# Performance work log

Measured on AMD Instinct MI355X. Metric: run time of the kernel, lower is better.

The kernel has to match this reference:

```python
import jax, jax.numpy as jnp
import numpy as np

# Capsule layer dims (from original CapsNet paper, per module docstring)
O = 10      # n_out_capsules
U = 36      # n_in_capsules_unique (6*6)
S = 32      # n_in_capsules_sharing_per_unique
E = 16      # n_out_features
F = 8       # n_in_features
N = U * S   # n_in_capsules = 1152
ITERS = 3   # n_iterations
B = 256     # batch size


def squash(v, axis):
    norm = jnp.linalg.norm(v, axis=axis, keepdims=True)
    return v * norm / (1.0 + norm ** 2)


def setup_inputs() -> dict:
    key = jax.random.key(0)
    k1, k2 = jax.random.split(key)
    x = jax.random.normal(k1, (B, N, F), dtype=jnp.float32)
    scale = np.float32(np.sqrt(2.0 / (N * F + O * E)))
    # weights: (n_out_capsules, n_in_capsules_unique, n_out_features, n_in_features)
    W = jax.random.normal(k2, (O, U, E, F), dtype=jnp.float32) * scale
    return {"x": x, "W": W}


def reference(x, W):
    b_sz = x.shape[0]
    xs = x.reshape(b_sz, U, S, F)
    # transform: shared weight over the S sharing dim -> (B, O, U, S, E)
    u = jnp.einsum('ouef,busf->bouse', W, xs).reshape(b_sz, O, N, E)
    u_hat = jax.lax.stop_gradient(u)

    b = jnp.zeros((b_sz, O, N), dtype=x.dtype)
    c = jax.nn.softmax(b, axis=1)  # uniform over output capsules
    for _ in range(ITERS):
        # v: (B, O, 1, E)
        v = squash(jnp.sum(c[..., None] * u_hat, axis=2, keepdims=True), axis=3)
        # agreement: (B, O, N)
        b = b + jnp.sum(u_hat * v, axis=3)
        c = jax.nn.softmax(b, axis=1)

    # final pass uses non-detached u so gradients flow through transform
    out = squash(jnp.sum(c[..., None] * u, axis=2, keepdims=True), axis=3)
    return out.reshape(b_sz, O, E)
```

## Files before the change

kernel.cpp:

```cpp
#include <hip/hip_runtime.h>
#include <math.h>


namespace {

constexpr int kO = 10;
constexpr int kU = 36;
constexpr int kS = 32;
constexpr int kE = 16;
constexpr int kF = 8;
constexpr int kN = kU * kS;
constexpr int kIters = 3;
constexpr int kThreads = 576;
constexpr int kRows = 2;
constexpr int kPitch = 12;

__launch_bounds__(kThreads, 2)
__global__ void caps_routing_kernel(const float* __restrict__ xg,
                                    const float* __restrict__ Wg,
                                    float* __restrict__ outg) {
    __shared__ float s_x[kN * kF];
    __shared__ float s_c[kO * kN];
    __shared__ float s_cx[kO * kU * kPitch];
    __shared__ float s_wv[kO * kU * kPitch];
    __shared__ float s_vp[kO * kE * 3];
    __shared__ float s_sx[kU * kF];

    const int t = threadIdx.x;
    const int b = blockIdx.x;

    float xr[kRows][kF];
    float br[kRows][kO];
    int   ru[kRows], rrot[kRows];

#pragma unroll
    for (int k = 0; k < kRows; ++k) {
        const int n = t + k * kThreads;
        const int u = n >> 5;
        const int s = n & 31;
        ru[k]   = u;
        rrot[k] = (s + u) & 31;
        const float4* src =
            reinterpret_cast<const float4*>(xg + ((size_t)b * kN + n) * kF);
        const float4 a0 = src[0];
        const float4 a1 = src[1];
        xr[k][0] = a0.x; xr[k][1] = a0.y; xr[k][2] = a0.z; xr[k][3] = a0.w;
        xr[k][4] = a1.x; xr[k][5] = a1.y; xr[k][6] = a1.z; xr[k][7] = a1.w;
        const int sl0 = ((s << 1) + 0 + u) & 63;
        const int sl1 = ((s << 1) + 1 + u) & 63;
        *reinterpret_cast<float4*>(&s_x[u * 256 + sl0 * 4]) = a0;
        *reinterpret_cast<float4*>(&s_x[u * 256 + sl1 * 4]) = a1;

        float4 r0 = a0, r1 = a1;
#pragma unroll
        for (int m = 1; m <= 16; m <<= 1) {
            r0.x += __shfl_xor(r0.x, m); r0.y += __shfl_xor(r0.y, m);
            r0.z += __shfl_xor(r0.z, m); r0.w += __shfl_xor(r0.w, m);
            r1.x += __shfl_xor(r1.x, m); r1.y += __shfl_xor(r1.y, m);
            r1.z += __shfl_xor(r1.z, m); r1.w += __shfl_xor(r1.w, m);
        }
        if (s == 0) {
            *reinterpret_cast<float4*>(&s_sx[u * kF + 0]) = r0;
            *reinterpret_cast<float4*>(&s_sx[u * kF + 4]) = r1;
        }
#pragma unroll
        for (int o = 0; o < kO; ++o) br[k][o] = 0.f;
    }
    __syncthreads();

    for (int it = 0; it <= kIters; ++it) {
        if (it > 0) {
            if (t < kO * kU) {
                const int o = t / kU;
                const int u = t - o * kU;
                float a0[kF] = {0, 0, 0, 0, 0, 0, 0, 0};
#pragma unroll 8
                for (int s = 0; s < kS; ++s) {
                    const int rot = (s + u) & 31;
                    const int sl0 = ((s << 1) + 0 + u) & 63;
                    const int sl1 = ((s << 1) + 1 + u) & 63;
                    const float4 xa =
                        *reinterpret_cast<const float4*>(&s_x[u * 256 + sl0 * 4]);
                    const float4 xb =
                        *reinterpret_cast<const float4*>(&s_x[u * 256 + sl1 * 4]);
                    const float c0 = s_c[o * kN + u * 32 + rot];
                    a0[0] += c0 * xa.x; a0[1] += c0 * xa.y;
                    a0[2] += c0 * xa.z; a0[3] += c0 * xa.w;
                    a0[4] += c0 * xb.x; a0[5] += c0 * xb.y;
                    a0[6] += c0 * xb.z; a0[7] += c0 * xb.w;
                }
                float4* d = reinterpret_cast<float4*>(&s_cx[(o * kU + u) * kPitch]);
                d[0] = make_float4(a0[0], a0[1], a0[2], a0[3]);
                d[1] = make_float4(a0[4], a0[5], a0[6], a0[7]);
            }
            __syncthreads();
        }

        if (t < kO * kE * 3) {
            const int o  = t / (kE * 3);
            const int r  = t - o * (kE * 3);
            const int e  = r / 3;
            const int uc = r - e * 3;
            const int u0 = uc * 12;
            float acc = 0.f;
            if (it == 0) {
                const float* wrow = Wg + ((size_t)(o * kU + u0) * kE + e) * kF;
#pragma unroll
                for (int ui = 0; ui < 12; ++ui) {
                    const float4* wp = reinterpret_cast<const float4*>(wrow);
                    const float4 w0 = wp[0];
                    const float4 w1 = wp[1];
                    const float4* cp =
                        reinterpret_cast<const float4*>(&s_sx[(u0 + ui) * kF]);
                    const float4 c0 = cp[0];
                    const float4 c1 = cp[1];
                    acc += w0.x * c0.x + w0.y * c0.y + w0.z * c0.z + w0.w * c0.w;
                    acc += w1.x * c1.x + w1.y * c1.y + w1.z * c1.z + w1.w * c1.w;
                    wrow += kE * kF;
                }
                acc *= 0.1f;
            } else {
                const float* wrow = Wg + ((size_t)(o * kU + u0) * kE + e) * kF;
#pragma unroll
                for (int ui = 0; ui < 12; ++ui) {
                    const float4* wp = reinterpret_cast<const float4*>(wrow);
                    const float4 w0 = wp[0];
                    const float4 w1 = wp[1];
                    const float4* cp = reinterpret_cast<const float4*>(
                        &s_cx[(o * kU + u0 + ui) * kPitch]);
                    const float4 c0 = cp[0];
                    const float4 c1 = cp[1];
                    acc += w0.x * c0.x + w0.y * c0.y + w0.z * c0.z + w0.w * c0.w;
                    acc += w1.x * c1.x + w1.y * c1.y + w1.z * c1.z + w1.w * c1.w;
                    wrow += kE * kF;
                }
            }
            s_vp[(o * kE + e) * 3 + uc] = acc;
        }
        __syncthreads();

        if (it == kIters) {
            if (t < kO * kE) {
                const float vsum = s_vp[t * 3 + 0] + s_vp[t * 3 + 1] + s_vp[t * 3 + 2];
                float n2 = vsum * vsum;
#pragma unroll
                for (int m = 1; m <= 8; m <<= 1) n2 += __shfl_xor(n2, m);
                const float scale = sqrtf(n2) / (1.f + n2);
                outg[(size_t)b * kO * kE + t] = vsum * scale;
            }
            break;
        }

        if (t < kO * kU) {
            const int o = t / kU;
            const int u = t - o * kU;
#define SUMVP(E_) (s_vp[(o * kE + (E_)) * 3 + 0] + \
                   s_vp[(o * kE + (E_)) * 3 + 1] + \
                   s_vp[(o * kE + (E_)) * 3 + 2])
            float4 va, vb, vc, vd;
            va.x = SUMVP(0);  va.y = SUMVP(1);  va.z = SUMVP(2);  va.w = SUMVP(3);
            vb.x = SUMVP(4);  vb.y = SUMVP(5);  vb.z = SUMVP(6);  vb.w = SUMVP(7);
            vc.x = SUMVP(8);  vc.y = SUMVP(9);  vc.z = SUMVP(10); vc.w = SUMVP(11);
            vd.x = SUMVP(12); vd.y = SUMVP(13); vd.z = SUMVP(14); vd.w = SUMVP(15);
#undef SUMVP
            const float n2 =
                va.x * va.x + va.y * va.y + va.z * va.z + va.w * va.w +
                vb.x * vb.x + vb.y * vb.y + vb.z * vb.z + vb.w * vb.w +
                vc.x * vc.x + vc.y * vc.y + vc.z * vc.z + vc.w * vc.w +
                vd.x * vd.x + vd.y * vd.y + vd.z * vd.z + vd.w * vd.w;
            const float scale = sqrtf(n2) / (1.f + n2);
            const float* wbase = Wg + (size_t)(o * kU + u) * kE * kF;
            float4 acc0 = make_float4(0.f, 0.f, 0.f, 0.f);
            float4 acc1 = make_float4(0.f, 0.f, 0.f, 0.f);
#define WSTEP(VE_, E_)                                                        \
    {                                                                         \
        const float4* wp =                                                    \
            reinterpret_cast<const float4*>(wbase + (E_) * kF);               \
        const float4 w0 = wp[0];                                              \
        const float4 w1 = wp[1];                                              \
        const float ve = (VE_) * scale;                                       \
        acc0.x += ve * w0.x; acc0.y += ve * w0.y;                             \
        acc0.z += ve * w0.z; acc0.w += ve * w0.w;                             \
        acc1.x += ve * w1.x; acc1.y += ve * w1.y;                             \
        acc1.z += ve * w1.z; acc1.w += ve * w1.w;                             \
    }
            WSTEP(va.x, 0)  WSTEP(va.y, 1)  WSTEP(va.z, 2)  WSTEP(va.w, 3)
            WSTEP(vb.x, 4)  WSTEP(vb.y, 5)  WSTEP(vb.z, 6)  WSTEP(vb.w, 7)
            WSTEP(vc.x, 8)  WSTEP(vc.y, 9)  WSTEP(vc.z, 10) WSTEP(vc.w, 11)
            WSTEP(vd.x, 12) WSTEP(vd.y, 13) WSTEP(vd.z, 14) WSTEP(vd.w, 15)
#undef WSTEP
            float4* d = reinterpret_cast<float4*>(&s_wv[(o * kU + u) * kPitch]);
            d[0] = acc0;
            d[1] = acc1;
        }
        __syncthreads();

#pragma unroll
        for (int k = 0; k < kRows; ++k) {
            const int u   = ru[k];
            const int rot = rrot[k];
            float mx = -3.4e38f;
#pragma unroll
            for (int o = 0; o < kO; ++o) {
                const float4* wp =
                    reinterpret_cast<const float4*>(&s_wv[(o * kU + u) * kPitch]);
                const float4 w0 = wp[0];
                const float4 w1 = wp[1];
                br[k][o] += w0.x * xr[k][0] + w0.y * xr[k][1] + w0.z * xr[k][2] + w0.w * xr[k][3]
                          + w1.x * xr[k][4] + w1.y * xr[k][5] + w1.z * xr[k][6] + w1.w * xr[k][7];
                mx = fmaxf(mx, br[k][o]);
            }
            float ex[kO];
            float sum = 0.f;
#pragma unroll
            for (int o = 0; o < kO; ++o) {
                ex[o] = __expf(br[k][o] - mx);
                sum += ex[o];
            }
            const float inv = 1.f / sum;
#pragma unroll
            for (int o = 0; o < kO; ++o) s_c[o * kN + u * 32 + rot] = ex[o] * inv;
        }
        __syncthreads();
    }
}

}

extern "C" void kernel_launch(void* const* d_in, const int* in_sizes, int n_in,
                              void* d_out, int out_size, void* d_ws, size_t ws_size,
                              hipStream_t stream) {
    const float* x = (const float*)d_in[0];
    const float* W = (const float*)d_in[1];
    float* out = (float*)d_out;

    const int batch = in_sizes[0] / (kN * kF);
    caps_routing_kernel<<<dim3(batch), dim3(kThreads), 0, stream>>>(x, W, out);
}
```

Before: 111.3 us.

## Rebalance work across 8 waves with 512 threads and split cx reduction

Reduces the block from 576 to 512 threads (8 full waves). Each phase is redistributed evenly across the waves: the per-row softmax handles 2 or 3 rows per thread, and the c·x reduction splits the S dimension in half across lane pairs, with two output capsules per thread and a shuffle to combine. The other phases are spread as 60, 45 and 46 active lanes per wave rather than taking contiguous thread ranges. The aim is to remove partially idle waves and the serial 32-step reduction on few threads, at the cost of uneven per-thread row counts and some extra shuffles and register pressure.

```diff
diff --git a/kernel.cpp b/kernel.cpp
--- a/kernel.cpp
+++ b/kernel.cpp
@@ -11,218 +11,253 @@
 constexpr int kF = 8;
 constexpr int kN = kU * kS;
 constexpr int kIters = 3;
-constexpr int kThreads = 576;
-constexpr int kRows = 2;
+constexpr int kThreads = 512;
 constexpr int kPitch = 12;
 
 __launch_bounds__(kThreads, 2)
 __global__ void caps_routing_kernel(const float* __restrict__ xg,
                                     const float* __restrict__ Wg,
                                     float* __restrict__ outg) {
-    __shared__ float s_x[kN * kF];
-    __shared__ float s_c[kO * kN];
-    __shared__ float s_cx[kO * kU * kPitch];
-    __shared__ float s_wv[kO * kU * kPitch];
-    __shared__ float s_vp[kO * kE * 3];
-    __shared__ float s_sx[kU * kF];
-
-    const int t = threadIdx.x;
-    const int b = blockIdx.x;
-
-    float xr[kRows][kF];
-    float br[kRows][kO];
-    int   ru[kRows], rrot[kRows];
-
+  __shared__ float s_x[kN * kF];
+  __shared__ float s_c[kO * kN];
+  __shared__ float s_cx[kO * kU * kPitch];
+  __shared__ float s_wv[kO * kU * kPitch];
+  __shared__ float s_vp[kO * kE * 3];
+  __shared__ float s_sx[kU * kF];
+
+  const int t = threadIdx.x;
+  const int w = t >> 6;
+  const int l = t & 63;
+  const int b = blockIdx.x;
+
+  float xr0[kF], xr1[kF], xr2[kF];
+  float br0[kO], br1[kO], br2[kO];
+  const bool has3 = (w < 4) && (l < 32);
+
+  const int u0r = t >> 5;
+  const int s0r = t & 31;
+  const int rot0 = (s0r + u0r) & 31;
+  const int u1r = 16 + (t >> 5);
+  const int rot1 = (s0r + u1r) & 31;
+  const int u2r = 32 + w;
+  const int rot2 = (l + u2r) & 31;
+
+#define STAGEROW(XR, N, U, S)                                                 \
+  {                                                                           \
+    const float4* src_ =                                                      \
+        reinterpret_cast<const float4*>(xg + ((size_t)b * kN + (N)) * kF);    \
+    const float4 a0_ = src_[0];                                               \
+    const float4 a1_ = src_[1];                                               \
+    XR[0] = a0_.x; XR[1] = a0_.y; XR[2] = a0_.z; XR[3] = a0_.w;               \
+    XR[4] = a1_.x; XR[5] = a1_.y; XR[6] = a1_.z; XR[7] = a1_.w;               \
+    const int sl0_ = (((S) << 1) + (U)) & 63;                                 \
+    const int sl1_ = (((S) << 1) + 1 + (U)) & 63;                             \
+    *reinterpret_cast<float4*>(&s_x[(U) * 256 + sl0_ * 4]) = a0_;             \
+    *reinterpret_cast<float4*>(&s_x[(U) * 256 + sl1_ * 4]) = a1_;             \
+    float4 r0_ = a0_, r1_ = a1_;                                              \
+    _Pragma("unroll")                                                         \
+    for (int m_ = 1; m_ <= 16; m_ <<= 1) {                                    \
+      r0_.x += __shfl_xor(r0_.x, m_); r0_.y += __shfl_xor(r0_.y, m_);         \
+      r0_.z += __shfl_xor(r0_.z, m_); r0_.w += __shfl_xor(r0_.w, m_);         \
+      r1_.x += __shfl_xor(r1_.x, m_); r1_.y += __shfl_xor(r1_.y, m_);         \
+      r1_.z += __shfl_xor(r1_.z, m_); r1_.w += __shfl_xor(r1_.w, m_);         \
+    }                                                                         \
+    if ((S) == 0) {                                                           \
+      *reinterpret_cast<float4*>(&s_sx[(U) * kF + 0]) = r0_;                  \
+      *reinterpret_cast<float4*>(&s_sx[(U) * kF + 4]) = r1_;                  \
+    }                                                                         \
+  }
+
+  STAGEROW(xr0, t, u0r, s0r)
+  STAGEROW(xr1, t + 512, u1r, s0r)
+  if (has3) STAGEROW(xr2, 1024 + w * 32 + l, u2r, l)
+#undef STAGEROW
 #pragma unroll
-    for (int k = 0; k < kRows; ++k) {
-        const int n = t + k * kThreads;
-        const int u = n >> 5;
-        const int s = n & 31;
-        ru[k]   = u;
-        rrot[k] = (s + u) & 31;
-        const float4* src =
-            reinterpret_cast<const float4*>(xg + ((size_t)b * kN + n) * kF);
-        const float4 a0 = src[0];
-        const float4 a1 = src[1];
-        xr[k][0] = a0.x; xr[k][1] = a0.y; xr[k][2] = a0.z; xr[k][3] = a0.w;
-        xr[k][4] = a1.x; xr[k][5] = a1.y; xr[k][6] = a1.z; xr[k][7] = a1.w;
-        const int sl0 = ((s << 1) + 0 + u) & 63;
-        const int sl1 = ((s << 1) + 1 + u) & 63;
-        *reinterpret_cast<float4*>(&s_x[u * 256 + sl0 * 4]) = a0;
-        *reinterpret_cast<float4*>(&s_x[u * 256 + sl1 * 4]) = a1;
-
-        float4 r0 = a0, r1 = a1;
+  for (int o = 0; o < kO; ++o) { br0[o] = 0.f; br1[o] = 0.f; br2[o] = 0.f; }
+  __syncthreads();
+
+  for (int it = 0; it <= kIters; ++it) {
+    if (it > 0) {
+      if (l < 46) {
+        const int i = w * 46 + l;
+        if (i < 360) {
+          const int op  = i / 72;
+          const int rem = i - op * 72;
+          const int u   = rem >> 1;
+          const int h   = rem & 1;
+          const int o0  = op * 2, o1 = o0 + 1;
+          float4 p00 = make_float4(0.f, 0.f, 0.f, 0.f);
+          float4 p01 = make_float4(0.f, 0.f, 0.f, 0.f);
+          float4 p10 = make_float4(0.f, 0.f, 0.f, 0.f);
+          float4 p11 = make_float4(0.f, 0.f, 0.f, 0.f);
+#pragma unroll 4
+          for (int j = 0; j < 16; ++j) {
+            const int s   = h * 16 + j;
+            const int rot = (s + u) & 31;
+            const int sl0 = ((s << 1) + u) & 63;
+            const int sl1 = ((s << 1) + 1 + u) & 63;
+            const float4 xa =
+                *reinterpret_cast<const float4*>(&s_x[u * 256 + sl0 * 4]);
+            const float4 xb =
+                *reinterpret_cast<const float4*>(&s_x[u * 256 + sl1 * 4]);
+            const float c0 = s_c[o0 * kN + u * 32 + rot];
+            const float c1 = s_c[o1 * kN + u * 32 + rot];
+            p00.x += c0 * xa.x; p00.y += c0 * xa.y; p00.z += c0 * xa.z; p00.w += c0 * xa.w;
+            p01.x += c0 * xb.x; p01.y += c0 * xb.y; p01.z += c0 * xb.z; p01.w += c0 * xb.w;
+            p10.x += c1 * xa.x; p10.y += c1 * xa.y; p10.z += c1 * xa.z; p10.w += c1 * xa.w;
+            p11.x += c1 * xb.x; p11.y += c1 * xb.y; p11.z += c1 * xb.z; p11.w += c1 * xb.w;
+          }
+          p00.x += __shfl_xor(p00.x, 1); p00.y += __shfl_xor(p00.y, 1);
+          p00.z += __shfl_xor(p00.z, 1); p00.w += __shfl_xor(p00.w, 1);
+          p01.x += __shfl_xor(p01.x, 1); p01.y += __shfl_xor(p01.y, 1);
+          p01.z += __shfl_xor(p01.z, 1); p01.w += __shfl_xor(p01.w, 1);
+          p10.x += __shfl_xor(p10.x, 1); p10.y += __shfl_xor(p10.y, 1);
+          p10.z += __shfl_xor(p10.z, 1); p10.w += __shfl_xor(p10.w, 1);
+          p11.x += __shfl_xor(p11.x, 1); p11.y += __shfl_xor(p11.y, 1);
+          p11.z += __shfl_xor(p11.z, 1); p11.w += __shfl_xor(p11.w, 1);
+          if (h == 0) {
+            float4* d = reinterpret_cast<float4*>(&s_cx[(o0 * kU + u) * kPitch]);
+            d[0] = p00; d[1] = p01;
+          } else {
+            float4* d = reinterpret_cast<float4*>(&s_cx[(o1 * kU + u) * kPitch]);
+            d[0] = p10; d[1] = p11;
+          }
+        }
+      }
+      __syncthreads();
+    }
+
+    if (l < 60) {
+      const int i  = w * 60 + l;
+      const int o  = i / 48;
+      const int r  = i - o * 48;
+      const int e  = r / 3;
+      const int uc = r - e * 3;
+      const int u0 = uc * 12;
+      float accA = 0.f, accB = 0.f;
+      const float* wrow = Wg + ((size_t)(o * kU + u0) * kE + e) * kF;
+      if (it == 0) {
+#pragma unroll 4
+        for (int ui = 0; ui < 12; ++ui) {
+          const float4* wp = reinterpret_cast<const float4*>(wrow);
+          const float4 w0 = wp[0];
+          const float4 w1 = wp[1];
+          const float4* cp =
+              reinterpret_cast<const float4*>(&s_sx[(u0 + ui) * kF]);
+          const float4 c0 = cp[0];
+          const float4 c1 = cp[1];
+          accA += w0.x * c0.x + w0.y * c0.y + w0.z * c0.z + w0.w * c0.w;
+          accB += w1.x * c1.x + w1.y * c1.y + w1.z * c1.z + w1.w * c1.w;
+          wrow += kE * kF;
+        }
+        accA = (accA + accB) * 0.1f;
+      } else {
+#pragma unroll 4
+        for (int ui = 0; ui < 12; ++ui) {
+          const float4* wp = reinterpret_cast<const float4*>(wrow);
+          const float4 w0 = wp[0];
+          const float4 w1 = wp[1];
+          const float4* cp = reinterpret_cast<const float4*>(
+              &s_cx[(o * kU + u0 + ui) * kPitch]);
+          const float4 c0 = cp[0];
+          const float4 c1 = cp[1];
+          accA += w0.x * c0.x + w0.y * c0.y + w0.z * c0.z + w0.w * c0.w;
+          accB += w1.x * c1.x + w1.y * c1.y + w1.z * c1.z + w1.w * c1.w;
+          wrow += kE * kF;
+        }
+        accA += accB;
+      }
+      s_vp[(o * kE + e) * 3 + uc] = accA;
+    }
+    __syncthreads();
+
+    if (it == kIters) {
+      if (t < kO * kE) {
+        const float vsum = s_vp[t * 3 + 0] + s_vp[t * 3 + 1] + s_vp[t * 3 + 2];
+        float n2 = vsum * vsum;
 #pragma unroll
-        for (int m = 1; m <= 16; m <<= 1) {
-            r0.x += __shfl_xor(r0.x, m); r0.y += __shfl_xor(r0.y, m);
-            r0.z += __shfl_xor(r0.z, m); r0.w += __shfl_xor(r0.w, m);
-            r1.x += __shfl_xor(r1.x, m); r1.y += __shfl_xor(r1.y, m);
-            r1.z += __shfl_xor(r1.z, m); r1.w += __shfl_xor(r1.w, m);
-        }
-        if (s == 0) {
-            *reinterpret_cast<float4*>(&s_sx[u * kF + 0]) = r0;
-            *reinterpret_cast<float4*>(&s_sx[u * kF + 4]) = r1;
-        }
-#pragma unroll
-        for (int o = 0; o < kO; ++o) br[k][o] = 0.f;
-    }
-    __syncthreads();
-
-    for (int it = 0; it <= kIters; ++it) {
-        if (it > 0) {
-            if (t < kO * kU) {
-                const int o = t / kU;
-                const int u = t - o * kU;
-                float a0[kF] = {0, 0, 0, 0, 0, 0, 0, 0};
-#pragma unroll 8
-                for (int s = 0; s < kS; ++s) {
-                    const int rot = (s + u) & 31;
-                    const int sl0 = ((s << 1) + 0 + u) & 63;
-                    const int sl1 = ((s << 1) + 1 + u) & 63;
-                    const float4 xa =
-                        *reinterpret_cast<const float4*>(&s_x[u * 256 + sl0 * 4]);
-                    const float4 xb =
-                        *reinterpret_cast<const float4*>(&s_x[u * 256 + sl1 * 4]);
-                    const float c0 = s_c[o * kN + u * 32 + rot];
-                    a0[0] += c0 * xa.x; a0[1] += c0 * xa.y;
-                    a0[2] += c0 * xa.z; a0[3] += c0 * xa.w;
-                    a0[4] += c0 * xb.x; a0[5] += c0 * xb.y;
-                    a0[6] += c0 * xb.z; a0[7] += c0 * xb.w;
-                }
-                float4* d = reinterpret_cast<float4*>(&s_cx[(o * kU + u) * kPitch]);
-                d[0] = make_float4(a0[0], a0[1], a0[2], a0[3]);
-                d[1] = make_float4(a0[4], a0[5], a0[6], a0[7]);
-            }
-            __syncthreads();
-        }
-
-        if (t < kO * kE * 3) {
-            const int o  = t / (kE * 3);
-            const int r  = t - o * (kE * 3);
-            const int e  = r / 3;
-            const int uc = r - e * 3;
-            const int u0 = uc * 12;
-            float acc = 0.f;
-            if (it == 0) {
-                const float* wrow = Wg + ((size_t)(o * kU + u0) * kE + e) * kF;
-#pragma unroll
-                for (int ui = 0; ui < 12; ++ui) {
-                    const float4* wp = reinterpret_cast<const float4*>(wrow);
-                    const float4 w0 = wp[0];
-                    const float4 w1 = wp[1];
-                    const float4* cp =
-                        reinterpret_cast<const float4*>(&s_sx[(u0 + ui) * kF]);
-                    const float4 c0 = cp[0];
-                    const float4 c1 = cp[1];
-                    acc += w0.x * c0.x + w0.y * c0.y + w0.z * c0.z + w0.w * c0.w;
-                    acc += w1.x * c1.x + w1.y * c1.y + w1.z * c1.z + w1.w * c1.w;
-                    wrow += kE * kF;
-                }
-                acc *= 0.1f;
-            } else {
-                const float* wrow = Wg + ((size_t)(o * kU + u0) * kE + e) * kF;
-#pragma unroll
-                for (int ui = 0; ui < 12; ++ui) {
-                    const float4* wp = reinterpret_cast<const float4*>(wrow);
-                    const float4 w0 = wp[0];
-                    const float4 w1 = wp[1];
-                    const float4* cp = reinterpret_cast<const float4*>(
-                        &s_cx[(o * kU + u0 + ui) * kPitch]);
-                    const float4 c0 = cp[0];
-                    const float4 c1 = cp[1];
-                    acc += w0.x * c0.x + w0.y * c0.y + w0.z * c0.z + w0.w * c0.w;
-                    acc += w1.x * c1.x + w1.y * c1.y + w1.z * c1.z + w1.w * c1.w;
-                    wrow += kE * kF;
-                }
-            }
-            s_vp[(o * kE + e) * 3 + uc] = acc;
-        }
-        __syncthreads();
-
-        if (it == kIters) {
-            if (t < kO * kE) {
-                const float vsum = s_vp[t * 3 + 0] + s_vp[t * 3 + 1] + s_vp[t * 3 + 2];
-                float n2 = vsum * vsum;
-#pragma unroll
-                for (int m = 1; m <= 8; m <<= 1) n2 += __shfl_xor(n2, m);
-                const float scale = sqrtf(n2) / (1.f + n2);
-                outg[(size_t)b * kO * kE + t] = vsum * scale;
-            }
-            break;
-        }
-
-        if (t < kO * kU) {
-            const int o = t / kU;
-            const int u = t - o * kU;
+        for (int m = 1; m <= 8; m <<= 1) n2 += __shfl_xor(n2, m);
+        const float scale = sqrtf(n2) / (1.f + n2);
+        outg[(size_t)b * kO * kE + t] = vsum * scale;
+      }
+      break;
+    }
+
+    if (l < 45) {
+      const int i = w * 45 + l;
+      const int o = i / 36;
+      const int u = i - o * 36;
 #define SUMVP(E_) (s_vp[(o * kE + (E_)) * 3 + 0] + \
                    s_vp[(o * kE + (E_)) * 3 + 1] + \
                    s_vp[(o * kE + (E_)) * 3 + 2])
-            float4 va, vb, vc, vd;
-            va.x = SUMVP(0);  va.y = SUMVP(1);  va.z = SUMVP(2);  va.w = SUMVP(3);
-            vb.x = SUMVP(4);  vb.y = SUMVP(5);  vb.z = SUMVP(6);  vb.w = SUMVP(7);
-            vc.x = SUMVP(8);  vc.y = SUMVP(9);  vc.z = SUMVP(10); vc.w = SUMVP(11);
-            vd.x = SUMVP(12); vd.y = SUMVP(13); vd.z = SUMVP(14); vd.w = SUMVP(15);
+      float4 va, vb, vc, vd;
+      va.x = SUMVP(0);  va.y = SUMVP(1);  va.z = SUMVP(2);  va.w = SUMVP(3);
+      vb.x = SUMVP(4);  vb.y = SUMVP(5);  vb.z = SUMVP(6);  vb.w = SUMVP(7);
+      vc.x = SUMVP(8);  vc.y = SUMVP(9);  vc.z = SUMVP(10); vc.w = SUMVP(11);
+      vd.x = SUMVP(12); vd.y = SUMVP(13); vd.z = SUMVP(14); vd.w = SUMVP(15);
 #undef SUMVP
-            const float n2 =
-                va.x * va.x + va.y * va.y + va.z * va.z + va.w * va.w +
-                vb.x * vb.x + vb.y * vb.y + vb.z * vb.z + vb.w * vb.w +
-                vc.x * vc.x + vc.y * vc.y + vc.z * vc.z + vc.w * vc.w +
-                vd.x * vd.x + vd.y * vd.y + vd.z * vd.z + vd.w * vd.w;
-            const float scale = sqrtf(n2) / (1.f + n2);
-            const float* wbase = Wg + (size_t)(o * kU + u) * kE * kF;
-            float4 acc0 = make_float4(0.f, 0.f, 0.f, 0.f);
-            float4 acc1 = make_float4(0.f, 0.f, 0.f, 0.f);
+      const float n2 =
+          va.x * va.x + va.y * va.y + va.z * va.z + va.w * va.w +
+          vb.x * vb.x + vb.y * vb.y + vb.z * vb.z + vb.w * vb.w +
+          vc.x * vc.x + vc.y * vc.y + vc.z * vc.z + vc.w * vc.w +
+          vd.x * vd.x + vd.y * vd.y + vd.z * vd.z + vd.w * vd.w;
+      const float scale = sqrtf(n2) / (1.f + n2);
+      const float* wbase = Wg + (size_t)(o * kU + u) * kE * kF;
+      float4 acc0 = make_float4(0.f, 0.f, 0.f, 0.f);
+      float4 acc1 = make_float4(0.f, 0.f, 0.f, 0.f);
 #define WSTEP(VE_, E_)                                                        \
-    {                                                                         \
-        const float4* wp =                                                    \
-            reinterpret_cast<const float4*>(wbase + (E_) * kF);               \
-        const float4 w0 = wp[0];                                              \
-        const float4 w1 = wp[1];                                              \
-        const float ve = (VE_) * scale;                                       \
-        acc0.x += ve * w0.x; acc0.y += ve * w0.y;                             \
-        acc0.z += ve * w0.z; acc0.w += ve * w0.w;                             \
-        acc1.x += ve * w1.x; acc1.y += ve * w1.y;                             \
-        acc1.z += ve * w1.z; acc1.w += ve * w1.w;                             \
-    }
-            WSTEP(va.x, 0)  WSTEP(va.y, 1)  WSTEP(va.z, 2)  WSTEP(va.w, 3)
-            WSTEP(vb.x, 4)  WSTEP(vb.y, 5)  WSTEP(vb.z, 6)  WSTEP(vb.w, 7)
-            WSTEP(vc.x, 8)  WSTEP(vc.y, 9)  WSTEP(vc.z, 10) WSTEP(vc.w, 11)
-            WSTEP(vd.x, 12) WSTEP(vd.y, 13) WSTEP(vd.z, 14) WSTEP(vd.w, 15)
+  {                                                                           \
+    const float4* wp = reinterpret_cast<const float4*>(wbase + (E_) * kF);    \
+    const float4 w0 = wp[0];                                                  \
+    const float4 w1 = wp[1];                                                  \
+    const float ve = (VE_) * scale;                                           \
+    acc0.x += ve * w0.x; acc0.y += ve * w0.y;                                 \
+    acc0.z += ve * w0.z; acc0.w += ve * w0.w;                                 \
+    acc1.x += ve * w1.x; acc1.y += ve * w1.y;                                 \
+    acc1.z += ve * w1.z; acc1.w += ve * w1.w;                                 \
+  }
+      WSTEP(va.x, 0)  WSTEP(va.y, 1)  WSTEP(va.z, 2)  WSTEP(va.w, 3)
+      WSTEP(vb.x, 4)  WSTEP(vb.y, 5)  WSTEP(vb.z, 6)  WSTEP(vb.w, 7)
+      WSTEP(vc.x, 8)  WSTEP(vc.y, 9)  WSTEP(vc.z, 10) WSTEP(vc.w, 11)
+      WSTEP(vd.x, 12) WSTEP(vd.y, 13) WSTEP(vd.z, 14) WSTEP(vd.w, 15)
 #undef WSTEP
-            float4* d = reinterpret_cast<float4*>(&s_wv[(o * kU + u) * kPitch]);
-            d[0] = acc0;
-            d[1] = acc1;
-        }
-        __syncthreads();
-
-#pragma unroll
-        for (int k = 0; k < kRows; ++k) {
-            const int u   = ru[k];
-            const int rot = rrot[k];
-            float mx = -3.4e38f;
-#pragma unroll
-            for (int o = 0; o < kO; ++o) {
-                const float4* wp =
-                    reinterpret_cast<const float4*>(&s_wv[(o * kU + u) * kPitch]);
-                const float4 w0 = wp[0];
-                const float4 w1 = wp[1];
-                br[k][o] += w0.x * xr[k][0] + w0.y * xr[k][1] + w0.z * xr[k][2] + w0.w * xr[k][3]
-                          + w1.x * xr[k][4] + w1.y * xr[k][5] + w1.z * xr[k][6] + w1.w * xr[k][7];
-                mx = fmaxf(mx, br[k][o]);
-            }
-            float ex[kO];
-            float sum = 0.f;
-#pragma unroll
-            for (int o = 0; o < kO; ++o) {
-                ex[o] = __expf(br[k][o] - mx);
-                sum += ex[o];
-            }
-            const float inv = 1.f / sum;
-#pragma unroll
-            for (int o = 0; o < kO; ++o) s_c[o * kN + u * 32 + rot] = ex[o] * inv;
-        }
-        __syncthreads();
-    }
+      float4* d = reinterpret_cast<float4*>(&s_wv[(o * kU + u) * kPitch]);
+      d[0] = acc0;
+      d[1] = acc1;
+    }
+    __syncthreads();
+
+#define BSMROW(XR, BR, U, ROT)                                                \
+  {                                                                           \
+    float mx_ = -3.4e38f;                                                     \
+    _Pragma("unroll")                                                         \
+    for (int o_ = 0; o_ < kO; ++o_) {                                         \
+      const float4* wp_ =                                                     \
+          reinterpret_cast<const float4*>(&s_wv[(o_ * kU + (U)) * kPitch]);   \
+      const float4 w0_ = wp_[0];                                              \
+      const float4 w1_ = wp_[1];                                              \
+      BR[o_] += w0_.x * XR[0] + w0_.y * XR[1] + w0_.z * XR[2] + w0_.w * XR[3] \
+              + w1_.x * XR[4] + w1_.y * XR[5] + w1_.z * XR[6] + w1_.w * XR[7];\
+      mx_ = fmaxf(mx_, BR[o_]);                                               \
+    }                                                                         \
+    float ex_[kO];                                                            \
+    float sum_ = 0.f;                                                         \
+    _Pragma("unroll")                                                         \
+    for (int o_ = 0; o_ < kO; ++o_) {                                         \
+      ex_[o_] = __expf(BR[o_] - mx_);                                         \
+      sum_ += ex_[o_];                                                        \
+    }                                                                         \
+    const float inv_ = 1.f / sum_;                                            \
+    _Pragma("unroll")                                                         \
+    for (int o_ = 0; o_ < kO; ++o_)                                           \
+      s_c[o_ * kN + (U) * 32 + (ROT)] = ex_[o_] * inv_;                       \
+  }
+    BSMROW(xr0, br0, u0r, rot0)
+    BSMROW(xr1, br1, u1r, rot1)
+    if (has3) BSMROW(xr2, br2, u2r, rot2)
+#undef BSMROW
+    __syncthreads();
+  }
 }
 
 }
@@ -230,10 +265,10 @@
 extern "C" void kernel_launch(void* const* d_in, const int* in_sizes, int n_in,
                               void* d_out, int out_size, void* d_ws, size_t ws_size,
                               hipStream_t stream) {
-    const float* x = (const float*)d_in[0];
-    const float* W = (const float*)d_in[1];
-    float* out = (float*)d_out;
-
-    const int batch = in_sizes[0] / (kN * kF);
-    caps_routing_kernel<<<dim3(batch), dim3(kThreads), 0, stream>>>(x, W, out);
+  const float* x = (const float*)d_in[0];
+  const float* W = (const float*)d_in[1];
+  float* out = (float*)d_out;
+
+  const int batch = in_sizes[0] / (kN * kF);
+  caps_routing_kernel<<<dim3(batch), dim3(kThreads), 0, stream>>>(x, W, out);
 }
```

Result: faster. 105.4 us (-5.3%).
